# Optimization experiments

Measured on AMD Instinct MI355X. Metric: run time of the kernel, lower is better.

The kernel has to match this reference:

```python
import jax, jax.numpy as jnp
import numpy as np

NEG_BIG = -1.0e9


def setup_inputs() -> dict:
    key = jax.random.key(0)
    ks = jax.random.split(key, 8)
    B, N, D = 4, 384, 256
    s = 1.0 / np.sqrt(D)
    return {
        "q": jax.random.normal(ks[0], (B, N, D), dtype=jnp.float32),
        "k": jax.random.normal(ks[1], (B, N, D), dtype=jnp.float32),
        "v": jax.random.normal(ks[2], (B, N, D), dtype=jnp.float32),
        "mask": jax.random.randint(ks[3], (B, 1, N, N), 0, 2, dtype=jnp.int32),
        "Wq": jax.random.normal(ks[4], (D, D), dtype=jnp.float32) * s,
        "bq": jnp.zeros((D,), dtype=jnp.float32),
        "Wk": jax.random.normal(ks[5], (D, D), dtype=jnp.float32) * s,
        "bk": jnp.zeros((D,), dtype=jnp.float32),
        "Wv": jax.random.normal(ks[6], (D, D), dtype=jnp.float32) * s,
        "bv": jnp.zeros((D,), dtype=jnp.float32),
    }


def reference(q, k, v, mask, Wq, bq, Wk, bk, Wv, bv):
    # Dense projections
    query = q @ Wq + bq   # [B, N, D]
    key_p = k @ Wk + bk   # [B, M, D]
    value = v @ Wv + bv   # [B, M, D]
    # Per-channel outer-product scores: [B, D, N, M]
    score = jnp.einsum('bnd,bmd->bdnm', query, key_p)
    score = score + mask.astype(score.dtype) * NEG_BIG  # mask broadcasts [B,1,N,M]
    weights = jnp.tanh(score)
    # Per-channel weighted sum back to [B, N, D]
    out = jnp.einsum('bdnm,bmd->bnd', weights, value)
    return out
```

## Files before the change

### kernel.cpp

```cpp
#include <hip/hip_runtime.h>

#define DD 256
#define NN 384
#define BB 4
#define BN (BB * NN)
#define MSPLIT 4
#define MCHUNK (NN / MSPLIT)
#define PSTRIDE (BN * DD)

constexpr float TWO_LOG2E = 2.8853900817779268f;

__global__ __launch_bounds__(256) void proj_kernel(
    const float* __restrict__ q,  const float* __restrict__ k,  const float* __restrict__ v,
    const float* __restrict__ Wq, const float* __restrict__ Wk, const float* __restrict__ Wv,
    const float* __restrict__ bq, const float* __restrict__ bk, const float* __restrict__ bv,
    float* __restrict__ Qout, float* __restrict__ KVout)
{
    const int tid  = threadIdx.x;
    const int row0 = blockIdx.x * 8;
    const int which = blockIdx.y;

    const float* X; const float* W; const float* bias; float scale; float* out; int ostride;
    if (which == 0)      { X = q; W = Wq; bias = bq; scale = 1.0f;      out = Qout;      ostride = 1; }
    else if (which == 1) { X = k; W = Wk; bias = bk; scale = TWO_LOG2E; out = KVout;     ostride = 2; }
    else                 { X = v; W = Wv; bias = bv; scale = 1.0f;      out = KVout + 1; ostride = 2; }

    const float* Xr = X + (size_t)row0 * DD;

    float acc[8] = {0.f,0.f,0.f,0.f,0.f,0.f,0.f,0.f};
    #pragma unroll 2
    for (int k0 = 0; k0 < DD; k0 += 4) {
        float w0 = W[(k0 + 0) * DD + tid];
        float w1 = W[(k0 + 1) * DD + tid];
        float w2 = W[(k0 + 2) * DD + tid];
        float w3 = W[(k0 + 3) * DD + tid];
        #pragma unroll
        for (int r = 0; r < 8; ++r) {
            acc[r] = fmaf(Xr[r * DD + k0 + 0], w0, acc[r]);
            acc[r] = fmaf(Xr[r * DD + k0 + 1], w1, acc[r]);
            acc[r] = fmaf(Xr[r * DD + k0 + 2], w2, acc[r]);
            acc[r] = fmaf(Xr[r * DD + k0 + 3], w3, acc[r]);
        }
    }
    const float bb = bias[tid];
    #pragma unroll
    for (int r = 0; r < 8; ++r)
        out[((row0 + r) * DD + tid) * ostride] = (acc[r] + bb) * scale;
}

__global__ __launch_bounds__(256, 6) void mhsa_kernel(
    const float* __restrict__ Q, const float* __restrict__ KV,
    const int* __restrict__ mask, float* __restrict__ outp)
{
    const int tid = threadIdx.x;
    const int b   = blockIdx.y;
    const int n0  = blockIdx.x * 4;
    const int m0  = blockIdx.z * MCHUNK;

    float qv[4];
    #pragma unroll
    for (int j = 0; j < 4; ++j)
        qv[j] = Q[(b * NN + n0 + j) * DD + tid];

    const int* mrow[4];
    #pragma unroll
    for (int j = 0; j < 4; ++j)
        mrow[j] = mask + (size_t)(b * NN + n0 + j) * NN + m0;

    const float2* kvp = reinterpret_cast<const float2*>(KV)
                      + (size_t)b * NN * DD + (size_t)m0 * DD + tid;

    float acc[4] = {0.f, 0.f, 0.f, 0.f};
    for (int mg = 0; mg < MCHUNK; mg += 4) {
        float2 kv[4];
        #pragma unroll
        for (int u = 0; u < 4; ++u)
            kv[u] = kvp[(size_t)(mg + u) * DD];
        #pragma unroll
        for (int u = 0; u < 4; ++u) {
            #pragma unroll
            for (int j = 0; j < 4; ++j) {
                if (mrow[j][mg + u]) {
                    acc[j] -= kv[u].y;
                } else {
                    const float x = qv[j] * kv[u].x;
                    const float E = __builtin_amdgcn_exp2f(x);
                    const float r = __builtin_amdgcn_rcpf(E + 1.0f);
                    acc[j] += fmaf(-2.0f * kv[u].y, r, kv[u].y);
                }
            }
        }
    }
    float* po = outp + (size_t)blockIdx.z * PSTRIDE;
    #pragma unroll
    for (int j = 0; j < 4; ++j)
        po[(b * NN + n0 + j) * DD + tid] = acc[j];
}

__global__ __launch_bounds__(256) void reduce4_kernel(
    const float* __restrict__ part, float* __restrict__ out)
{
    const int i = blockIdx.x * 256 + threadIdx.x;
    out[i] = (part[i] + part[i + PSTRIDE])
           + (part[i + 2 * PSTRIDE] + part[i + 3 * PSTRIDE]);
}

extern "C" void kernel_launch(void* const* d_in, const int* in_sizes, int n_in,
                              void* d_out, int out_size, void* d_ws, size_t ws_size,
                              hipStream_t stream) {
    const float* q    = (const float*)d_in[0];
    const float* k    = (const float*)d_in[1];
    const float* v    = (const float*)d_in[2];
    const int*   mask = (const int*)  d_in[3];
    const float* Wq   = (const float*)d_in[4];
    const float* bq   = (const float*)d_in[5];
    const float* Wk   = (const float*)d_in[6];
    const float* bk   = (const float*)d_in[7];
    const float* Wv   = (const float*)d_in[8];
    const float* bv   = (const float*)d_in[9];
    float* out = (float*)d_out;

    float* Qws   = (float*)d_ws;
    float* KVws  = Qws  + (size_t)BN * DD;
    float* Pws   = KVws + (size_t)2 * BN * DD;

    dim3 g1(BN / 8, 3);
    proj_kernel<<<g1, 256, 0, stream>>>(q, k, v, Wq, Wk, Wv, bq, bk, bv, Qws, KVws);

    dim3 g2(NN / 4, BB, MSPLIT);
    mhsa_kernel<<<g2, 256, 0, stream>>>(Qws, KVws, mask, Pws);

    reduce4_kernel<<<dim3(BN * DD / 256), 256, 0, stream>>>(Pws, out);
}
```

Before: 145.9 us.

## Make masking branchless, hoist value sum, double-buffer KV loads, tile projection

The attention kernel stages the mask into shared memory as an additive exponent bias, which removes the per-element branch and the wave divergence it causes. The value term is summed once per m and added at the end, so each inner step needs one FMA instead of two. KV loads are double-buffered in groups of eight to hide memory latency. The projection kernel now splits K across its four waves, stages X in shared memory, uses float4 weight loads with prefetch and reduces the partial sums in shared memory. The cost is extra shared memory, added synchronisation, and exp2 evaluated on masked entries as well.

```diff
diff --git a/kernel.cpp b/kernel.cpp
--- a/kernel.cpp
+++ b/kernel.cpp
@@ -9,6 +9,7 @@
 #define PSTRIDE (BN * DD)
 
 constexpr float TWO_LOG2E = 2.8853900817779268f;
+constexpr float MASK_X    = -1.0e9f * 2.8853900817779268f;
 
 __global__ __launch_bounds__(256) void proj_kernel(
     const float* __restrict__ q,  const float* __restrict__ k,  const float* __restrict__ v,
@@ -17,6 +18,8 @@
     float* __restrict__ Qout, float* __restrict__ KVout)
 {
     const int tid  = threadIdx.x;
+    const int lane = tid & 63;
+    const int wv   = tid >> 6;
     const int row0 = blockIdx.x * 8;
     const int which = blockIdx.y;
 
@@ -25,27 +28,69 @@
     else if (which == 1) { X = k; W = Wk; bias = bk; scale = TWO_LOG2E; out = KVout;     ostride = 2; }
     else                 { X = v; W = Wv; bias = bv; scale = 1.0f;      out = KVout + 1; ostride = 2; }
 
-    const float* Xr = X + (size_t)row0 * DD;
-
-    float acc[8] = {0.f,0.f,0.f,0.f,0.f,0.f,0.f,0.f};
-    #pragma unroll 2
-    for (int k0 = 0; k0 < DD; k0 += 4) {
-        float w0 = W[(k0 + 0) * DD + tid];
-        float w1 = W[(k0 + 1) * DD + tid];
-        float w2 = W[(k0 + 2) * DD + tid];
-        float w3 = W[(k0 + 3) * DD + tid];
+    __shared__ float xs[DD][8];
+    __shared__ float ps[4][8][DD];
+
+    const float* Xb = X + (size_t)row0 * DD;
+    for (int e = tid; e < 8 * DD; e += 256) {
+        const int r  = e >> 8;
+        const int kk = e & 255;
+        xs[kk][r] = Xb[e];
+    }
+    __syncthreads();
+
+    const int k0 = wv * 64;
+    const float* Wp = W + (size_t)k0 * DD + lane * 4;
+
+    float4 acc[8];
+    #pragma unroll
+    for (int r = 0; r < 8; ++r) acc[r] = make_float4(0.f, 0.f, 0.f, 0.f);
+
+    float4 wbuf[4];
+    #pragma unroll
+    for (int i = 0; i < 4; ++i) wbuf[i] = *reinterpret_cast<const float4*>(Wp + (size_t)i * DD);
+
+    #pragma unroll 4
+    for (int kk = 0; kk < 60; ++kk) {
+        const float4 w4 = wbuf[kk & 3];
+        wbuf[kk & 3] = *reinterpret_cast<const float4*>(Wp + (size_t)(kk + 4) * DD);
+        const float4 xa = *reinterpret_cast<const float4*>(&xs[k0 + kk][0]);
+        const float4 xb = *reinterpret_cast<const float4*>(&xs[k0 + kk][4]);
+        const float xr[8] = {xa.x, xa.y, xa.z, xa.w, xb.x, xb.y, xb.z, xb.w};
         #pragma unroll
         for (int r = 0; r < 8; ++r) {
-            acc[r] = fmaf(Xr[r * DD + k0 + 0], w0, acc[r]);
-            acc[r] = fmaf(Xr[r * DD + k0 + 1], w1, acc[r]);
-            acc[r] = fmaf(Xr[r * DD + k0 + 2], w2, acc[r]);
-            acc[r] = fmaf(Xr[r * DD + k0 + 3], w3, acc[r]);
+            acc[r].x = fmaf(xr[r], w4.x, acc[r].x);
+            acc[r].y = fmaf(xr[r], w4.y, acc[r].y);
+            acc[r].z = fmaf(xr[r], w4.z, acc[r].z);
+            acc[r].w = fmaf(xr[r], w4.w, acc[r].w);
         }
     }
-    const float bb = bias[tid];
+    #pragma unroll
+    for (int kk = 60; kk < 64; ++kk) {
+        const float4 w4 = wbuf[kk & 3];
+        const float4 xa = *reinterpret_cast<const float4*>(&xs[k0 + kk][0]);
+        const float4 xb = *reinterpret_cast<const float4*>(&xs[k0 + kk][4]);
+        const float xr[8] = {xa.x, xa.y, xa.z, xa.w, xb.x, xb.y, xb.z, xb.w};
+        #pragma unroll
+        for (int r = 0; r < 8; ++r) {
+            acc[r].x = fmaf(xr[r], w4.x, acc[r].x);
+            acc[r].y = fmaf(xr[r], w4.y, acc[r].y);
+            acc[r].z = fmaf(xr[r], w4.z, acc[r].z);
+            acc[r].w = fmaf(xr[r], w4.w, acc[r].w);
+        }
+    }
+
     #pragma unroll
     for (int r = 0; r < 8; ++r)
-        out[((row0 + r) * DD + tid) * ostride] = (acc[r] + bb) * scale;
+        *reinterpret_cast<float4*>(&ps[wv][r][lane * 4]) = acc[r];
+    __syncthreads();
+
+    for (int e = tid; e < 8 * DD; e += 256) {
+        const int r = e >> 8;
+        const int d = e & 255;
+        const float s = (ps[0][r][d] + ps[1][r][d]) + (ps[2][r][d] + ps[3][r][d]);
+        out[((size_t)(row0 + r) * DD + d) * ostride] = (s + bias[d]) * scale;
+    }
 }
 
 __global__ __launch_bounds__(256, 6) void mhsa_kernel(
@@ -57,44 +102,68 @@
     const int n0  = blockIdx.x * 4;
     const int m0  = blockIdx.z * MCHUNK;
 
+    __shared__ float mf[MCHUNK][4];
+    for (int idx = tid; idx < MCHUNK * 4; idx += 256) {
+        const int m = idx % MCHUNK;
+        const int j = idx / MCHUNK;
+        mf[m][j] = mask[(size_t)(b * NN + n0 + j) * NN + (m0 + m)] ? MASK_X : 0.0f;
+    }
+    __syncthreads();
+
     float qv[4];
     #pragma unroll
     for (int j = 0; j < 4; ++j)
-        qv[j] = Q[(b * NN + n0 + j) * DD + tid];
-
-    const int* mrow[4];
-    #pragma unroll
-    for (int j = 0; j < 4; ++j)
-        mrow[j] = mask + (size_t)(b * NN + n0 + j) * NN + m0;
+        qv[j] = Q[(size_t)(b * NN + n0 + j) * DD + tid];
 
     const float2* kvp = reinterpret_cast<const float2*>(KV)
                       + (size_t)b * NN * DD + (size_t)m0 * DD + tid;
 
     float acc[4] = {0.f, 0.f, 0.f, 0.f};
-    for (int mg = 0; mg < MCHUNK; mg += 4) {
-        float2 kv[4];
-        #pragma unroll
-        for (int u = 0; u < 4; ++u)
-            kv[u] = kvp[(size_t)(mg + u) * DD];
-        #pragma unroll
-        for (int u = 0; u < 4; ++u) {
+    float vsum = 0.f;
+
+#define PROJ_COMPUTE(MLOC, KVV)                                          \
+    {                                                                    \
+        const float4 m4 = *reinterpret_cast<const float4*>(&mf[MLOC][0]);\
+        const float kk = (KVV).x, vv = (KVV).y;                          \
+        const float t2 = -2.0f * vv;                                     \
+        vsum += vv;                                                      \
+        const float mm[4] = {m4.x, m4.y, m4.z, m4.w};                    \
+        _Pragma("unroll")                                                \
+        for (int j = 0; j < 4; ++j) {                                    \
+            const float x = fmaf(qv[j], kk, mm[j]);                      \
+            const float E = __builtin_amdgcn_exp2f(x);                   \
+            const float r = __builtin_amdgcn_rcpf(E + 1.0f);             \
+            acc[j] = fmaf(t2, r, acc[j]);                                \
+        }                                                                \
+    }
+
+    float2 bufA[8], bufB[8];
+    #pragma unroll
+    for (int u = 0; u < 8; ++u)
+        bufA[u] = kvp[(size_t)u * DD];
+
+    for (int mg = 0; mg < MCHUNK; mg += 16) {
+        #pragma unroll
+        for (int u = 0; u < 8; ++u)
+            bufB[u] = kvp[(size_t)(mg + 8 + u) * DD];
+        #pragma unroll
+        for (int u = 0; u < 8; ++u)
+            PROJ_COMPUTE(mg + u, bufA[u]);
+        if (mg + 16 < MCHUNK) {
             #pragma unroll
-            for (int j = 0; j < 4; ++j) {
-                if (mrow[j][mg + u]) {
-                    acc[j] -= kv[u].y;
-                } else {
-                    const float x = qv[j] * kv[u].x;
-                    const float E = __builtin_amdgcn_exp2f(x);
-                    const float r = __builtin_amdgcn_rcpf(E + 1.0f);
-                    acc[j] += fmaf(-2.0f * kv[u].y, r, kv[u].y);
-                }
-            }
+            for (int u = 0; u < 8; ++u)
+                bufA[u] = kvp[(size_t)(mg + 16 + u) * DD];
         }
-    }
+        #pragma unroll
+        for (int u = 0; u < 8; ++u)
+            PROJ_COMPUTE(mg + 8 + u, bufB[u]);
+    }
+#undef PROJ_COMPUTE
+
     float* po = outp + (size_t)blockIdx.z * PSTRIDE;
     #pragma unroll
     for (int j = 0; j < 4; ++j)
-        po[(b * NN + n0 + j) * DD + tid] = acc[j];
+        po[(size_t)(b * NN + n0 + j) * DD + tid] = acc[j] + vsum;
 }
 
 __global__ __launch_bounds__(256) void reduce4_kernel(
```

Measured after the change: 152.1 us. +4.2%, slower.

## Make masked attention branchless and split-K the projection GEMM with float4 tiles

Applied to the files above, without the earlier changes.

The attention kernel stages the mask for its four query rows into shared memory as an additive large negative bias. This removes the per-element divergent branch on the random mask. The v term is factored into a running vsum so each element costs one FMA per accumulator, and KV loads are software-pipelined with double register buffers. The projection kernel splits K across the four waves with float4 loads and 4-wide outputs per lane, then reduces the partials through shared memory. The pipelined loads read past the chunk on the last iteration; those values are unused but land in adjacent workspace memory.

```diff
diff --git a/kernel.cpp b/kernel.cpp
--- a/kernel.cpp
+++ b/kernel.cpp
@@ -9,6 +9,7 @@
 #define PSTRIDE (BN * DD)
 
 constexpr float TWO_LOG2E = 2.8853900817779268f;
+constexpr float MASK_X    = -1.0e9f * 2.8853900817779268f;
 
 __global__ __launch_bounds__(256) void proj_kernel(
     const float* __restrict__ q,  const float* __restrict__ k,  const float* __restrict__ v,
@@ -17,6 +18,8 @@
     float* __restrict__ Qout, float* __restrict__ KVout)
 {
     const int tid  = threadIdx.x;
+    const int lane = tid & 63;
+    const int wv   = tid >> 6;
     const int row0 = blockIdx.x * 8;
     const int which = blockIdx.y;
 
@@ -25,30 +28,55 @@
     else if (which == 1) { X = k; W = Wk; bias = bk; scale = TWO_LOG2E; out = KVout;     ostride = 2; }
     else                 { X = v; W = Wv; bias = bv; scale = 1.0f;      out = KVout + 1; ostride = 2; }
 
-    const float* Xr = X + (size_t)row0 * DD;
+    __shared__ float ps[4][8][DD];
 
-    float acc[8] = {0.f,0.f,0.f,0.f,0.f,0.f,0.f,0.f};
+    const int k0 = wv * 64;
+    const float* Xb = X + (size_t)row0 * DD + k0;
+    const float* Wp = W + (size_t)k0 * DD + lane * 4;
+
+    float4 acc[8];
+    #pragma unroll
+    for (int r = 0; r < 8; ++r) acc[r] = make_float4(0.f, 0.f, 0.f, 0.f);
+
     #pragma unroll 2
-    for (int k0 = 0; k0 < DD; k0 += 4) {
-        float w0 = W[(k0 + 0) * DD + tid];
-        float w1 = W[(k0 + 1) * DD + tid];
-        float w2 = W[(k0 + 2) * DD + tid];
-        float w3 = W[(k0 + 3) * DD + tid];
+    for (int g = 0; g < 16; ++g) {
+        float4 xq[8];
         #pragma unroll
-        for (int r = 0; r < 8; ++r) {
-            acc[r] = fmaf(Xr[r * DD + k0 + 0], w0, acc[r]);
-            acc[r] = fmaf(Xr[r * DD + k0 + 1], w1, acc[r]);
-            acc[r] = fmaf(Xr[r * DD + k0 + 2], w2, acc[r]);
-            acc[r] = fmaf(Xr[r * DD + k0 + 3], w3, acc[r]);
+        for (int r = 0; r < 8; ++r)
+            xq[r] = *reinterpret_cast<const float4*>(Xb + r * DD + g * 4);
+        float4 wq[4];
+        #pragma unroll
+        for (int u = 0; u < 4; ++u)
+            wq[u] = *reinterpret_cast<const float4*>(Wp + (size_t)(g * 4 + u) * DD);
+        #pragma unroll
+        for (int u = 0; u < 4; ++u) {
+            const float4 w = wq[u];
+            #pragma unroll
+            for (int r = 0; r < 8; ++r) {
+                const float x = (u == 0) ? xq[r].x : (u == 1) ? xq[r].y
+                              : (u == 2) ? xq[r].z : xq[r].w;
+                acc[r].x = fmaf(x, w.x, acc[r].x);
+                acc[r].y = fmaf(x, w.y, acc[r].y);
+                acc[r].z = fmaf(x, w.z, acc[r].z);
+                acc[r].w = fmaf(x, w.w, acc[r].w);
+            }
         }
     }
-    const float bb = bias[tid];
+
     #pragma unroll
     for (int r = 0; r < 8; ++r)
-        out[((row0 + r) * DD + tid) * ostride] = (acc[r] + bb) * scale;
+        *reinterpret_cast<float4*>(&ps[wv][r][lane * 4]) = acc[r];
+    __syncthreads();
+
+    for (int e = tid; e < 8 * DD; e += 256) {
+        const int r = e >> 8;
+        const int d = e & 255;
+        const float s = (ps[0][r][d] + ps[1][r][d]) + (ps[2][r][d] + ps[3][r][d]);
+        out[((size_t)(row0 + r) * DD + d) * ostride] = (s + bias[d]) * scale;
+    }
 }
 
-__global__ __launch_bounds__(256, 6) void mhsa_kernel(
+__global__ __launch_bounds__(256) void mhsa_kernel(
     const float* __restrict__ Q, const float* __restrict__ KV,
     const int* __restrict__ mask, float* __restrict__ outp)
 {
@@ -57,44 +85,64 @@
     const int n0  = blockIdx.x * 4;
     const int m0  = blockIdx.z * MCHUNK;
 
-    float qv[4];
-    #pragma unroll
-    for (int j = 0; j < 4; ++j)
-        qv[j] = Q[(b * NN + n0 + j) * DD + tid];
+    __shared__ float mf[MCHUNK][4];
+    for (int idx = tid; idx < MCHUNK * 4; idx += 256) {
+        const int m = idx % MCHUNK;
+        const int j = idx / MCHUNK;
+        mf[m][j] = mask[(size_t)(b * NN + n0 + j) * NN + (m0 + m)] ? MASK_X : 0.0f;
+    }
+    __syncthreads();
 
-    const int* mrow[4];
-    #pragma unroll
-    for (int j = 0; j < 4; ++j)
-        mrow[j] = mask + (size_t)(b * NN + n0 + j) * NN + m0;
+    float qv0 = Q[(size_t)(b * NN + n0 + 0) * DD + tid];
+    float qv1 = Q[(size_t)(b * NN + n0 + 1) * DD + tid];
+    float qv2 = Q[(size_t)(b * NN + n0 + 2) * DD + tid];
+    float qv3 = Q[(size_t)(b * NN + n0 + 3) * DD + tid];
 
     const float2* kvp = reinterpret_cast<const float2*>(KV)
                       + (size_t)b * NN * DD + (size_t)m0 * DD + tid;
 
-    float acc[4] = {0.f, 0.f, 0.f, 0.f};
-    for (int mg = 0; mg < MCHUNK; mg += 4) {
-        float2 kv[4];
-        #pragma unroll
-        for (int u = 0; u < 4; ++u)
-            kv[u] = kvp[(size_t)(mg + u) * DD];
-        #pragma unroll
-        for (int u = 0; u < 4; ++u) {
-            #pragma unroll
-            for (int j = 0; j < 4; ++j) {
-                if (mrow[j][mg + u]) {
-                    acc[j] -= kv[u].y;
-                } else {
-                    const float x = qv[j] * kv[u].x;
-                    const float E = __builtin_amdgcn_exp2f(x);
-                    const float r = __builtin_amdgcn_rcpf(E + 1.0f);
-                    acc[j] += fmaf(-2.0f * kv[u].y, r, kv[u].y);
-                }
-            }
-        }
+    float acc0 = 0.f, acc1 = 0.f, acc2 = 0.f, acc3 = 0.f, vsum = 0.f;
+
+#define COMP(KVV, MLOC)                                                       \
+    {                                                                         \
+        const float4 m4 = *reinterpret_cast<const float4*>(&mf[MLOC][0]);     \
+        const float kk = (KVV).x, vv = (KVV).y;                               \
+        const float t2 = -2.0f * vv;                                          \
+        vsum += vv;                                                           \
+        const float x0 = fmaf(qv0, kk, m4.x);                                 \
+        const float x1 = fmaf(qv1, kk, m4.y);                                 \
+        const float x2 = fmaf(qv2, kk, m4.z);                                 \
+        const float x3 = fmaf(qv3, kk, m4.w);                                 \
+        acc0 = fmaf(t2, __builtin_amdgcn_rcpf(__builtin_amdgcn_exp2f(x0) + 1.0f), acc0); \
+        acc1 = fmaf(t2, __builtin_amdgcn_rcpf(__builtin_amdgcn_exp2f(x1) + 1.0f), acc1); \
+        acc2 = fmaf(t2, __builtin_amdgcn_rcpf(__builtin_amdgcn_exp2f(x2) + 1.0f), acc2); \
+        acc3 = fmaf(t2, __builtin_amdgcn_rcpf(__builtin_amdgcn_exp2f(x3) + 1.0f), acc3); \
     }
+
+#define LOADG(B0, B1, B2, B3, M0)                \
+    B0 = kvp[(size_t)((M0) + 0) * DD];           \
+    B1 = kvp[(size_t)((M0) + 1) * DD];           \
+    B2 = kvp[(size_t)((M0) + 2) * DD];           \
+    B3 = kvp[(size_t)((M0) + 3) * DD];
+
+    float2 A0, A1, A2, A3, B0, B1, B2, B3;
+    LOADG(A0, A1, A2, A3, 0)
+    LOADG(B0, B1, B2, B3, 4)
+
+    for (int mg = 0; mg < MCHUNK; mg += 8) {
+        COMP(A0, mg + 0) COMP(A1, mg + 1) COMP(A2, mg + 2) COMP(A3, mg + 3)
+        LOADG(A0, A1, A2, A3, mg + 8)
+        COMP(B0, mg + 4) COMP(B1, mg + 5) COMP(B2, mg + 6) COMP(B3, mg + 7)
+        LOADG(B0, B1, B2, B3, mg + 12)
+    }
+#undef COMP
+#undef LOADG
+
     float* po = outp + (size_t)blockIdx.z * PSTRIDE;
-    #pragma unroll
-    for (int j = 0; j < 4; ++j)
-        po[(b * NN + n0 + j) * DD + tid] = acc[j];
+    po[(size_t)(b * NN + n0 + 0) * DD + tid] = acc0 + vsum;
+    po[(size_t)(b * NN + n0 + 1) * DD + tid] = acc1 + vsum;
+    po[(size_t)(b * NN + n0 + 2) * DD + tid] = acc2 + vsum;
+    po[(size_t)(b * NN + n0 + 3) * DD + tid] = acc3 + vsum;
 }
 
 __global__ __launch_bounds__(256) void reduce4_kernel(
```

Measured after the change: 129.5 us. -11.3%, faster.
